# Optimization experiments

Hardware: AMD Instinct MI355X
Metric: run time of the kernel (lower is better)

## Reference

```python
import jax, jax.numpy as jnp
import numpy as np

N, E, G = 100000, 1600000, 500
F_IN, H, OUT, MD = 128, 128, 1, 30


def gcn_conv(x, src, dst, ew, W, b):
    # PyG GCNConv: x' = D^-1/2 (A + I) D^-1/2 (x W) + b, with edge weights ew
    n = x.shape[0]
    h = x @ W  # [N, H]
    loops = jnp.arange(n)
    s = jnp.concatenate([src, loops])
    d = jnp.concatenate([dst, loops])
    w = jnp.concatenate([ew, jnp.ones((n,), dtype=x.dtype)])
    deg = jax.ops.segment_sum(w, d, num_segments=n)
    dinv = jnp.where(deg > 0, jax.lax.rsqrt(deg), 0.0).astype(x.dtype)
    norm = dinv[s] * w * dinv[d]  # [E+N]
    out = jax.ops.segment_sum(norm[:, None] * h[s], d, num_segments=n)
    return out + b


def setup_inputs() -> dict:
    key = jax.random.key(0)
    ks = jax.random.split(key, 12)
    x = jax.random.normal(ks[0], (N, F_IN), dtype=jnp.float32)
    edge_index = jax.random.randint(ks[1], (2, E), 0, N, dtype=jnp.int64)
    edge_attr = jax.random.uniform(ks[2], (E,), dtype=jnp.float32)
    batch = jnp.sort(jax.random.randint(ks[3], (N,), 0, G, dtype=jnp.int64))
    metadata = jax.random.normal(ks[4], (G, MD), dtype=jnp.float32)
    s = lambda fi, fo: 1.0 / np.sqrt(fi)
    W1 = jax.random.normal(ks[5], (F_IN, H), dtype=jnp.float32) * s(F_IN, H)
    b1 = jnp.zeros((H,), dtype=jnp.float32)
    W2 = jax.random.normal(ks[6], (H, H), dtype=jnp.float32) * s(H, H)
    b2 = jnp.zeros((H,), dtype=jnp.float32)
    Wm = jax.random.normal(ks[7], (MD, H), dtype=jnp.float32) * s(MD, H)
    bm = jnp.zeros((H,), dtype=jnp.float32)
    Wf = jax.random.normal(ks[8], (2 * H, OUT), dtype=jnp.float32) * s(2 * H, OUT)
    bf = jnp.zeros((OUT,), dtype=jnp.float32)
    return {"x": x, "edge_index": edge_index, "edge_attr": edge_attr,
            "batch": batch, "metadata": metadata,
            "W1": W1, "b1": b1, "W2": W2, "b2": b2,
            "Wm": Wm, "bm": bm, "Wf": Wf, "bf": bf}


def reference(x, edge_index, edge_attr, batch, metadata, W1, b1, W2, b2, Wm, bm, Wf, bf):
    src, dst = edge_index[0], edge_index[1]
    h = jax.nn.relu(gcn_conv(x, src, dst, edge_attr, W1, b1))
    h = jax.nn.relu(gcn_conv(h, src, dst, edge_attr, W2, b2))
    # global_mean_pool over batch ids
    sums = jax.ops.segment_sum(h, batch, num_segments=G)
    cnt = jax.ops.segment_sum(jnp.ones((h.shape[0],), h.dtype), batch, num_segments=G)
    pooled = sums / jnp.maximum(cnt, 1.0)[:, None]  # [G, H]
    # per-graph metadata: first node index of graph i, idx = first_node % M
    first_node = jax.ops.segment_min(jnp.arange(batch.shape[0]), batch, num_segments=G)
    idx = first_node % metadata.shape[0]
    md = metadata[idx]  # [G, MD]
    md = jax.nn.relu(md @ Wm + bm)  # dropout inactive at eval
    z = jnp.concatenate([pooled, md], axis=1)
    return z @ Wf + bf
```

## Files before the change

kernel.cpp:

```cpp
#include <hip/hip_runtime.h>
#include <cstdint>


#define BK_SHIFT 9
#define BK_NODES 512
#define CH 4096
#define NODE_BITS 17
#define NODE_MASK ((1 << NODE_BITS) - 1)

typedef short bf16x8 __attribute__((ext_vector_type(8)));
typedef float f32x4 __attribute__((ext_vector_type(4)));

union bfpack {
    uint4 u;
    bf16x8 b;
};

static __device__ __forceinline__ unsigned int f2bf(float f) {
    unsigned int u = __float_as_uint(f);
    return (u + 0x7fffu + ((u >> 16) & 1u)) >> 16;
}
static __device__ __forceinline__ unsigned int packbf2(float a, float b) {
    return f2bf(a) | (f2bf(b) << 16);
}
static __device__ __forceinline__ float bf_lo(unsigned int v) {
    return __uint_as_float(v << 16);
}
static __device__ __forceinline__ float bf_hi(unsigned int v) {
    return __uint_as_float(v & 0xffff0000u);
}

__global__ void k_init_small(int* gstart, int* gend, int G, int* bcnt, int NBK) {
    int g = blockIdx.x * blockDim.x + threadIdx.x;
    if (g < G) { gstart[g] = 0x7fffffff; gend[g] = 0; }
    if (g < NBK) bcnt[g] = 0;
}

__global__ void k_init_nodes(const int* __restrict__ batch,
                             int* __restrict__ gstart, int* __restrict__ gend, int N) {
    int i = blockIdx.x * blockDim.x + threadIdx.x;
    if (i >= N) return;
    int b = batch[i];
    if (i == 0 || batch[i - 1] != b) gstart[b] = i;
    if (i == N - 1 || batch[i + 1] != b) gend[b] = i + 1;
}

__global__ __launch_bounds__(256) void k_binhist(const int* __restrict__ dst, int E,
                                                 int* __restrict__ bcnt, int NBK) {
    __shared__ int h[256];
    int tid = threadIdx.x;
    h[tid] = 0;
    __syncthreads();
    int base = blockIdx.x * CH;
    int nend = min(base + CH, E);
    for (int i = base + tid; i < nend; i += 256) atomicAdd(&h[dst[i] >> BK_SHIFT], 1);
    __syncthreads();
    if (tid < NBK && h[tid]) atomicAdd(&bcnt[tid], h[tid]);
}

__global__ __launch_bounds__(256) void k_binscan(const int* __restrict__ bcnt,
                                                 int* __restrict__ bbase,
                                                 int* __restrict__ bfill, int NBK) {
    __shared__ int sc[256];
    int tid = threadIdx.x;
    int v = (tid < NBK) ? bcnt[tid] : 0;
    sc[tid] = v;
    __syncthreads();
    for (int d = 1; d < 256; d <<= 1) {
        int t = (tid >= d) ? sc[tid - d] : 0;
        __syncthreads();
        sc[tid] += t;
        __syncthreads();
    }
    int excl = sc[tid] - v;
    if (tid < NBK) { bbase[tid] = excl; bfill[tid] = excl; }
    if (tid == 255) bbase[NBK] = sc[255];
}

__global__ __launch_bounds__(256) void k_binscatter(const int* __restrict__ src,
                                                    const int* __restrict__ dst,
                                                    const float* __restrict__ ew,
                                                    int* __restrict__ bfill,
                                                    int2* __restrict__ binned, int E) {
    __shared__ int2 stage2[CH];
    __shared__ unsigned char bkt2[CH];
    __shared__ int hist[256], sc[256], lofs[256], cnt2[256], gbase[256];
    int tid = threadIdx.x;
    int base = blockIdx.x * CH;
    int n = min(CH, E - base);
    hist[tid] = 0;
    cnt2[tid] = 0;
    __syncthreads();
    int2 ev[CH / 256];
    int bk[CH / 256];
#pragma unroll
    for (int j = 0; j < CH / 256; ++j) {
        int i = base + tid + j * 256;
        bk[j] = -1;
        if (i < base + n) {
            int s = src[i], d = dst[i];
            float w = ew[i];
            int b = d >> BK_SHIFT;
            ev[j] = make_int2(s | ((d & (BK_NODES - 1)) << NODE_BITS), __float_as_int(w));
            bk[j] = b;
            atomicAdd(&hist[b], 1);
        }
    }
    __syncthreads();
    int hv = hist[tid];
    sc[tid] = hv;
    __syncthreads();
    for (int d = 1; d < 256; d <<= 1) {
        int t = (tid >= d) ? sc[tid - d] : 0;
        __syncthreads();
        sc[tid] += t;
        __syncthreads();
    }
    lofs[tid] = sc[tid] - hv;
    gbase[tid] = hv ? atomicAdd(&bfill[tid], hv) : 0;
    __syncthreads();
#pragma unroll
    for (int j = 0; j < CH / 256; ++j) {
        if (bk[j] >= 0) {
            int r = atomicAdd(&cnt2[bk[j]], 1);
            int p = lofs[bk[j]] + r;
            stage2[p] = ev[j];
            bkt2[p] = (unsigned char)bk[j];
        }
    }
    __syncthreads();
    for (int i = tid; i < n; i += 256) {
        int b = bkt2[i];
        binned[gbase[b] + (i - lofs[b])] = stage2[i];
    }
}

__global__ __launch_bounds__(256) void k_csr(const int2* __restrict__ binned,
                                             const int* __restrict__ bbase,
                                             int2* __restrict__ cvb,
                                             int* __restrict__ rowptr,
                                             float* __restrict__ dinv, int N, int E) {
    __shared__ int lh[BK_NODES];
    __shared__ float ls[BK_NODES];
    __shared__ int lofs[BK_NODES];
    __shared__ int s2[256];
    int tid = threadIdx.x;
    int b = blockIdx.x;
    int nbase = b << BK_SHIFT;
    int nend = min(nbase + BK_NODES, N);
    int ebase = bbase[b], eend = bbase[b + 1];
    for (int i = tid; i < BK_NODES; i += 256) { lh[i] = 0; ls[i] = 0.f; }
    __syncthreads();
    for (int e = ebase + tid; e < eend; e += 256) {
        int2 v = binned[e];
        int local = (v.x >> NODE_BITS) & (BK_NODES - 1);
        atomicAdd(&lh[local], 1);
        atomicAdd(&ls[local], __int_as_float(v.y));
    }
    __syncthreads();
    int p0 = lh[2 * tid], p1 = lh[2 * tid + 1];
    int pv = p0 + p1;
    s2[tid] = pv;
    __syncthreads();
    for (int d = 1; d < 256; d <<= 1) {
        int t = (tid >= d) ? s2[tid - d] : 0;
        __syncthreads();
        s2[tid] += t;
        __syncthreads();
    }
    int e2 = s2[tid] - pv;
    lofs[2 * tid] = e2;
    lofs[2 * tid + 1] = e2 + p0;
    __syncthreads();
    for (int i = nbase + tid; i < nend; i += 256) {
        int local = i - nbase;
        rowptr[i] = ebase + lofs[local];
        dinv[i] = rsqrtf(1.0f + ls[local]);
    }
    if (b == 0 && tid == 0) rowptr[N] = E;
    __syncthreads();
    for (int e = ebase + tid; e < eend; e += 256) {
        int2 v = binned[e];
        int local = (v.x >> NODE_BITS) & (BK_NODES - 1);
        int r = atomicAdd(&lofs[local], 1);
        cvb[ebase + r] = make_int2(v.x & NODE_MASK, v.y);
    }
}

__global__ __launch_bounds__(256) void k_wtboth(const float* __restrict__ W1,
                                                const float* __restrict__ W2,
                                                unsigned short* __restrict__ WT1,
                                                unsigned short* __restrict__ WT2) {
    int idx = blockIdx.x * 256 + threadIdx.x;
    const float* W = (idx < 16384) ? W1 : W2;
    unsigned short* WT = (idx < 16384) ? WT1 : WT2;
    int i = idx & 16383;
    int n = i >> 7, k = i & 127;
    WT[i] = (unsigned short)f2bf(W[(size_t)k * 128 + n]);
}

__global__ __launch_bounds__(256) void k_gemm1(const float* __restrict__ X,
                                               const unsigned short* __restrict__ WT,
                                               const float* __restrict__ dinv,
                                               unsigned short* __restrict__ Y, int M) {
    int tid = threadIdx.x;
    int wid = tid >> 6, lane = tid & 63;
    int rowb = blockIdx.x * 64 + wid * 16;
    int r16 = lane & 15, kg = lane >> 4;
    int arow = min(rowb + r16, M - 1);
    const float* xr = X + (size_t)arow * 128 + kg * 8;
    bf16x8 a[4];
#pragma unroll
    for (int kc = 0; kc < 4; ++kc) {
        float4 u = *reinterpret_cast<const float4*>(xr + kc * 32);
        float4 v = *reinterpret_cast<const float4*>(xr + kc * 32 + 4);
        bfpack pk;
        pk.u = make_uint4(packbf2(u.x, u.y), packbf2(u.z, u.w),
                          packbf2(v.x, v.y), packbf2(v.z, v.w));
        a[kc] = pk.b;
    }
    float dv[4];
#pragma unroll
    for (int r = 0; r < 4; ++r) {
        int ro = rowb + kg * 4 + r;
        dv[r] = (ro < M) ? dinv[ro] : 0.f;
    }
    const bf16x8* Bp = reinterpret_cast<const bf16x8*>(WT + (size_t)r16 * 128 + kg * 8);
#pragma unroll
    for (int nt = 0; nt < 8; ++nt) {
        const bf16x8* B = Bp + (size_t)nt * 256;
        f32x4 acc = {0.f, 0.f, 0.f, 0.f};
        acc = __builtin_amdgcn_mfma_f32_16x16x32_bf16(a[0], B[0], acc, 0, 0, 0);
        acc = __builtin_amdgcn_mfma_f32_16x16x32_bf16(a[1], B[4], acc, 0, 0, 0);
        acc = __builtin_amdgcn_mfma_f32_16x16x32_bf16(a[2], B[8], acc, 0, 0, 0);
        acc = __builtin_amdgcn_mfma_f32_16x16x32_bf16(a[3], B[12], acc, 0, 0, 0);
        int colo = nt * 16 + r16;
#pragma unroll
        for (int r = 0; r < 4; ++r) {
            int ro = rowb + kg * 4 + r;
            if (ro < M) Y[(size_t)ro * 128 + colo] = (unsigned short)f2bf(acc[r] * dv[r]);
        }
    }
}

__global__ __launch_bounds__(256) void k_aggemm(const uint2* __restrict__ Hb2,
                                                const int* __restrict__ rowptr,
                                                const int2* __restrict__ cvb,
                                                const float* __restrict__ dinv,
                                                const float* __restrict__ bias,
                                                const unsigned short* __restrict__ WT2,
                                                unsigned short* __restrict__ Y, int N) {
    __shared__ int2 lcv[4][4][2][64];
    __shared__ uint2 hst[32][33];
    int tid = threadIdx.x;
    int lane = tid & 63, wid = tid >> 6;
    int half = lane >> 5, sl = lane & 31;
    int blockbase = blockIdx.x * 32;
    int n0 = blockbase + wid * 8;
    bool active = (n0 < N);
    float a[4][4];
#pragma unroll
    for (int s = 0; s < 4; ++s)
#pragma unroll
        for (int q = 0; q < 4; ++q) a[s][q] = 0.f;
    if (active) {
        int rv = rowptr[min(n0 + min(lane, 8), N)];
        int rp[9];
#pragma unroll
        for (int k = 0; k < 9; ++k) rp[k] = __shfl(rv, k);
        int cnt[8];
        int nmax = 0;
#pragma unroll
        for (int k = 0; k < 8; ++k) {
            cnt[k] = rp[k + 1] - rp[k];
            nmax = max(nmax, cnt[k]);
        }
#pragma unroll
        for (int s = 0; s < 4; ++s) {
            int ns = n0 + 2 * s + half;
            uint2 hv = (ns < N) ? Hb2[(size_t)ns * 32 + sl] : make_uint2(0u, 0u);
            a[s][0] = bf_lo(hv.x);
            a[s][1] = bf_hi(hv.x);
            a[s][2] = bf_lo(hv.y);
            a[s][3] = bf_hi(hv.y);
        }
        for (int base = 0; base < nmax; base += 64) {
#pragma unroll
            for (int s = 0; s < 4; ++s) {
#pragma unroll
                for (int h = 0; h < 2; ++h) {
                    int k = 2 * s + h;
                    int2 t = (base + lane < cnt[k]) ? cvb[rp[k] + base + lane]
                                                    : make_int2(0, 0);
                    lcv[wid][s][h][lane] = t;
                }
            }
            int m = min(64, nmax - base);
            for (int j0 = 0; j0 < m; j0 += 8) {
#pragma unroll
                for (int jj = 0; jj < 8; ++jj) {
                    int j = j0 + jj;
                    if (j < m) {
                        int2 e0 = lcv[wid][0][half][j];
                        int2 e1 = lcv[wid][1][half][j];
                        int2 e2 = lcv[wid][2][half][j];
                        int2 e3 = lcv[wid][3][half][j];
                        uint2 h0 = Hb2[(size_t)e0.x * 32 + sl];
                        uint2 h1 = Hb2[(size_t)e1.x * 32 + sl];
                        uint2 h2 = Hb2[(size_t)e2.x * 32 + sl];
                        uint2 h3 = Hb2[(size_t)e3.x * 32 + sl];
                        float w0 = __int_as_float(e0.y);
                        float w1 = __int_as_float(e1.y);
                        float w2 = __int_as_float(e2.y);
                        float w3 = __int_as_float(e3.y);
                        a[0][0] = fmaf(w0, bf_lo(h0.x), a[0][0]);
                        a[0][1] = fmaf(w0, bf_hi(h0.x), a[0][1]);
                        a[0][2] = fmaf(w0, bf_lo(h0.y), a[0][2]);
                        a[0][3] = fmaf(w0, bf_hi(h0.y), a[0][3]);
                        a[1][0] = fmaf(w1, bf_lo(h1.x), a[1][0]);
                        a[1][1] = fmaf(w1, bf_hi(h1.x), a[1][1]);
                        a[1][2] = fmaf(w1, bf_lo(h1.y), a[1][2]);
                        a[1][3] = fmaf(w1, bf_hi(h1.y), a[1][3]);
                        a[2][0] = fmaf(w2, bf_lo(h2.x), a[2][0]);
                        a[2][1] = fmaf(w2, bf_hi(h2.x), a[2][1]);
                        a[2][2] = fmaf(w2, bf_lo(h2.y), a[2][2]);
                        a[2][3] = fmaf(w2, bf_hi(h2.y), a[2][3]);
                        a[3][0] = fmaf(w3, bf_lo(h3.x), a[3][0]);
                        a[3][1] = fmaf(w3, bf_hi(h3.x), a[3][1]);
                        a[3][2] = fmaf(w3, bf_lo(h3.y), a[3][2]);
                        a[3][3] = fmaf(w3, bf_hi(h3.y), a[3][3]);
                    }
                }
            }
        }
    }
    float4 bv = reinterpret_cast<const float4*>(bias)[sl];
#pragma unroll
    for (int s = 0; s < 4; ++s) {
        int ns = n0 + 2 * s + half;
        uint2 o = make_uint2(0u, 0u);
        if (active && ns < N) {
            float d = dinv[ns];
            float o0 = fmaxf(fmaf(a[s][0], d, bv.x), 0.f);
            float o1 = fmaxf(fmaf(a[s][1], d, bv.y), 0.f);
            float o2 = fmaxf(fmaf(a[s][2], d, bv.z), 0.f);
            float o3 = fmaxf(fmaf(a[s][3], d, bv.w), 0.f);
            o = make_uint2(packbf2(o0, o1), packbf2(o2, o3));
        }
        hst[wid * 8 + 2 * s + half][sl] = o;
    }
    __syncthreads();
    int r16 = lane & 15, kg = lane >> 4;
    int trow = wid >> 1;
    int ntb = (wid & 1) * 4;
    int arow = trow * 16 + r16;
    bf16x8 afr[4];
#pragma unroll
    for (int kc = 0; kc < 4; ++kc) {
        uint2 lo = hst[arow][kc * 8 + kg * 2];
        uint2 hi = hst[arow][kc * 8 + kg * 2 + 1];
        bfpack pk;
        pk.u = make_uint4(lo.x, lo.y, hi.x, hi.y);
        afr[kc] = pk.b;
    }
    float dv[4];
#pragma unroll
    for (int r = 0; r < 4; ++r) {
        int ro = blockbase + trow * 16 + kg * 4 + r;
        dv[r] = (ro < N) ? dinv[ro] : 0.f;
    }
    const bf16x8* Bp = reinterpret_cast<const bf16x8*>(WT2 + (size_t)r16 * 128 + kg * 8);
#pragma unroll
    for (int nt = 0; nt < 4; ++nt) {
        const bf16x8* B = Bp + (size_t)(ntb + nt) * 256;
        f32x4 acc = {0.f, 0.f, 0.f, 0.f};
        acc = __builtin_amdgcn_mfma_f32_16x16x32_bf16(afr[0], B[0], acc, 0, 0, 0);
        acc = __builtin_amdgcn_mfma_f32_16x16x32_bf16(afr[1], B[4], acc, 0, 0, 0);
        acc = __builtin_amdgcn_mfma_f32_16x16x32_bf16(afr[2], B[8], acc, 0, 0, 0);
        acc = __builtin_amdgcn_mfma_f32_16x16x32_bf16(afr[3], B[12], acc, 0, 0, 0);
        int colo = (ntb + nt) * 16 + r16;
#pragma unroll
        for (int r = 0; r < 4; ++r) {
            int ro = blockbase + trow * 16 + kg * 4 + r;
            if (ro < N) Y[(size_t)ro * 128 + colo] = (unsigned short)f2bf(acc[r] * dv[r]);
        }
    }
}

__global__ __launch_bounds__(256) void k_agg(const uint2* __restrict__ Hb2,
                                             const int* __restrict__ rowptr,
                                             const int2* __restrict__ cvb,
                                             const float* __restrict__ dinv,
                                             const float* __restrict__ bias,
                                             uint2* __restrict__ OutB2, int N) {
    __shared__ int2 lcv[4][4][2][64];
    int tid = threadIdx.x;
    int lane = tid & 63, wid = tid >> 6;
    int half = lane >> 5, sl = lane & 31;
    int n0 = (blockIdx.x * 4 + wid) * 8;
    if (n0 >= N) return;
    int rv = rowptr[min(n0 + min(lane, 8), N)];
    int rp[9];
#pragma unroll
    for (int k = 0; k < 9; ++k) rp[k] = __shfl(rv, k);
    int cnt[8];
    int nmax = 0;
#pragma unroll
    for (int k = 0; k < 8; ++k) {
        cnt[k] = rp[k + 1] - rp[k];
        nmax = max(nmax, cnt[k]);
    }
    float a[4][4];
#pragma unroll
    for (int s = 0; s < 4; ++s) {
        int ns = n0 + 2 * s + half;
        uint2 hv = (ns < N) ? Hb2[(size_t)ns * 32 + sl] : make_uint2(0u, 0u);
        a[s][0] = bf_lo(hv.x);
        a[s][1] = bf_hi(hv.x);
        a[s][2] = bf_lo(hv.y);
        a[s][3] = bf_hi(hv.y);
    }
    for (int base = 0; base < nmax; base += 64) {
#pragma unroll
        for (int s = 0; s < 4; ++s) {
#pragma unroll
            for (int h = 0; h < 2; ++h) {
                int k = 2 * s + h;
                int2 t = (base + lane < cnt[k]) ? cvb[rp[k] + base + lane]
                                                : make_int2(0, 0);
                lcv[wid][s][h][lane] = t;
            }
        }
        int m = min(64, nmax - base);
        for (int j0 = 0; j0 < m; j0 += 8) {
#pragma unroll
            for (int jj = 0; jj < 8; ++jj) {
                int j = j0 + jj;
                if (j < m) {
                    int2 e0 = lcv[wid][0][half][j];
                    int2 e1 = lcv[wid][1][half][j];
                    int2 e2 = lcv[wid][2][half][j];
                    int2 e3 = lcv[wid][3][half][j];
                    uint2 h0 = Hb2[(size_t)e0.x * 32 + sl];
                    uint2 h1 = Hb2[(size_t)e1.x * 32 + sl];
                    uint2 h2 = Hb2[(size_t)e2.x * 32 + sl];
                    uint2 h3 = Hb2[(size_t)e3.x * 32 + sl];
                    float w0 = __int_as_float(e0.y);
                    float w1 = __int_as_float(e1.y);
                    float w2 = __int_as_float(e2.y);
                    float w3 = __int_as_float(e3.y);
                    a[0][0] = fmaf(w0, bf_lo(h0.x), a[0][0]);
                    a[0][1] = fmaf(w0, bf_hi(h0.x), a[0][1]);
                    a[0][2] = fmaf(w0, bf_lo(h0.y), a[0][2]);
                    a[0][3] = fmaf(w0, bf_hi(h0.y), a[0][3]);
                    a[1][0] = fmaf(w1, bf_lo(h1.x), a[1][0]);
                    a[1][1] = fmaf(w1, bf_hi(h1.x), a[1][1]);
                    a[1][2] = fmaf(w1, bf_lo(h1.y), a[1][2]);
                    a[1][3] = fmaf(w1, bf_hi(h1.y), a[1][3]);
                    a[2][0] = fmaf(w2, bf_lo(h2.x), a[2][0]);
                    a[2][1] = fmaf(w2, bf_hi(h2.x), a[2][1]);
                    a[2][2] = fmaf(w2, bf_lo(h2.y), a[2][2]);
                    a[2][3] = fmaf(w2, bf_hi(h2.y), a[2][3]);
                    a[3][0] = fmaf(w3, bf_lo(h3.x), a[3][0]);
                    a[3][1] = fmaf(w3, bf_hi(h3.x), a[3][1]);
                    a[3][2] = fmaf(w3, bf_lo(h3.y), a[3][2]);
                    a[3][3] = fmaf(w3, bf_hi(h3.y), a[3][3]);
                }
            }
        }
    }
    float4 bv = reinterpret_cast<const float4*>(bias)[sl];
#pragma unroll
    for (int s = 0; s < 4; ++s) {
        int ns = n0 + 2 * s + half;
        if (ns < N) {
            float d = dinv[ns];
            float o0 = fmaxf(fmaf(a[s][0], d, bv.x), 0.f);
            float o1 = fmaxf(fmaf(a[s][1], d, bv.y), 0.f);
            float o2 = fmaxf(fmaf(a[s][2], d, bv.z), 0.f);
            float o3 = fmaxf(fmaf(a[s][3], d, bv.w), 0.f);
            OutB2[(size_t)ns * 32 + sl] = make_uint2(packbf2(o0, o1), packbf2(o2, o3));
        }
    }
}

__global__ __launch_bounds__(256) void k_poolhead(const unsigned int* __restrict__ H2u,
                                                  const int* __restrict__ gstart,
                                                  const int* __restrict__ gend,
                                                  const float* __restrict__ meta,
                                                  const float* __restrict__ Wm,
                                                  const float* __restrict__ bm,
                                                  const float* __restrict__ Wf,
                                                  const float* __restrict__ bf,
                                                  float* __restrict__ out, int G) {
    int g = blockIdx.x;
    int tid = threadIdx.x;
    int cu = tid & 63, q = tid >> 6;
    __shared__ float r0[256], r1[256];
    __shared__ float pooled[128];
    __shared__ float red[128];
    int b = gstart[g];
    int e = gend[g];
    int cntg = e - b;
    float s0 = 0.f, s1 = 0.f;
    for (int i = q; i < cntg; i += 4) {
        unsigned int v = H2u[(size_t)(b + i) * 64 + cu];
        s0 += bf_lo(v);
        s1 += bf_hi(v);
    }
    r0[tid] = s0; r1[tid] = s1;
    __syncthreads();
    if (tid < 64) {
        float t0 = r0[cu] + r0[cu + 64] + r0[cu + 128] + r0[cu + 192];
        float t1 = r1[cu] + r1[cu + 64] + r1[cu + 128] + r1[cu + 192];
        float inv = 1.f / fmaxf((float)cntg, 1.f);
        pooled[2 * cu] = t0 * inv;
        pooled[2 * cu + 1] = t1 * inv;
    }
    __syncthreads();
    if (tid < 128) {
        int c = tid;
        int idx = gstart[g] % G;
        float m = bm[c];
#pragma unroll
        for (int k = 0; k < 30; ++k) m = fmaf(meta[idx * 30 + k], Wm[k * 128 + c], m);
        m = fmaxf(m, 0.f);
        red[c] = pooled[c] * Wf[c] + m * Wf[128 + c];
    }
    __syncthreads();
    for (int st = 64; st > 0; st >>= 1) {
        if (tid < st) red[tid] += red[tid + st];
        __syncthreads();
    }
    if (tid == 0) out[g] = red[0] + bf[0];
}

extern "C" void kernel_launch(void* const* d_in, const int* in_sizes, int n_in,
                              void* d_out, int out_size, void* d_ws, size_t ws_size,
                              hipStream_t stream) {
    const float* x     = (const float*)d_in[0];
    const int*   ei    = (const int*)d_in[1];
    const float* ew    = (const float*)d_in[2];
    const int*   batch = (const int*)d_in[3];
    const float* meta  = (const float*)d_in[4];
    const float* W1    = (const float*)d_in[5];
    const float* b1    = (const float*)d_in[6];
    const float* W2    = (const float*)d_in[7];
    const float* b2    = (const float*)d_in[8];
    const float* Wm    = (const float*)d_in[9];
    const float* bm    = (const float*)d_in[10];
    const float* Wf    = (const float*)d_in[11];
    const float* bf    = (const float*)d_in[12];

    int N = in_sizes[0] / 128;
    int E = in_sizes[2];
    int G = in_sizes[4] / 30;
    int Mpad = (N + 63) & ~63;
    int NBK = (N + BK_NODES - 1) >> BK_SHIFT;
    const int* srcp = ei;
    const int* dstp = ei + E;

    char* p = (char*)d_ws;
    auto alloc = [&](size_t bytes) -> void* {
        void* r = p;
        p += (bytes + 255) & ~(size_t)255;
        return r;
    };
    float* dinv   = (float*)alloc((size_t)N * 4);
    int*   rowptr = (int*)alloc((size_t)(N + 1) * 4);
    int2*  binned = (int2*)alloc((size_t)E * 8);
    int2*  cvb    = (int2*)alloc((size_t)E * 8);
    int*   bcnt   = (int*)alloc((size_t)NBK * 4);
    int*   bbase  = (int*)alloc((size_t)(NBK + 1) * 4);
    int*   bfillp = (int*)alloc((size_t)NBK * 4);
    unsigned short* H   = (unsigned short*)alloc((size_t)Mpad * 128 * 2);
    unsigned short* H2  = (unsigned short*)alloc((size_t)Mpad * 128 * 2);
    unsigned short* WT1 = (unsigned short*)alloc(128 * 128 * 2);
    unsigned short* WT2 = (unsigned short*)alloc(128 * 128 * 2);
    int*   gstart = (int*)alloc((size_t)G * 4);
    int*   gend   = (int*)alloc((size_t)G * 4);

    int EB = (E + CH - 1) / CH;
    k_init_small<<<(max(G, NBK) + 255) / 256, 256, 0, stream>>>(gstart, gend, G, bcnt, NBK);
    k_init_nodes<<<(N + 255) / 256, 256, 0, stream>>>(batch, gstart, gend, N);
    k_binhist<<<EB, 256, 0, stream>>>(dstp, E, bcnt, NBK);
    k_binscan<<<1, 256, 0, stream>>>(bcnt, bbase, bfillp, NBK);
    k_binscatter<<<EB, 256, 0, stream>>>(srcp, dstp, ew, bfillp, binned, E);
    k_csr<<<NBK, 256, 0, stream>>>(binned, bbase, cvb, rowptr, dinv, N, E);

    k_wtboth<<<128, 256, 0, stream>>>(W1, W2, WT1, WT2);

    k_gemm1<<<Mpad / 64, 256, 0, stream>>>(x, WT1, dinv, H, N);
    int NB32 = (N + 31) / 32;
    k_aggemm<<<NB32, 256, 0, stream>>>((const uint2*)H, rowptr, cvb, dinv, b1, WT2,
                                       H2, N);
    k_agg<<<NB32, 256, 0, stream>>>((const uint2*)H2, rowptr, cvb, dinv, b2,
                                    (uint2*)H, N);

    k_poolhead<<<G, 256, 0, stream>>>((const unsigned int*)H, gstart, gend,
                                      meta, Wm, bm, Wf, bf, (float*)d_out, G);
}
```

Baseline: 290.9 us.

## Make fused aggregate-GEMM per-wave to drop block barrier; privatize histogram per wave

The fused aggregation+GEMM kernel now has each wave work independently: it stages its own 8 rows in a per-wave shared buffer, reused for both edge lists and output staging, and runs the 16x16 MFMA with half the rows zero-padded over all 8 column tiles. This removes the __syncthreads and lets waves with no work exit early, so one slow wave no longer holds the others up. In exchange, half of every MFMA's work is wasted on padding and each wave issues twice as many MFMAs. The bin histogram also gets per-wave shared-memory copies to cut atomic contention.

```diff
diff --git a/kernel.cpp b/kernel.cpp
--- a/kernel.cpp
+++ b/kernel.cpp
@@ -47,15 +47,20 @@
 
 __global__ __launch_bounds__(256) void k_binhist(const int* __restrict__ dst, int E,
                                                  int* __restrict__ bcnt, int NBK) {
-    __shared__ int h[256];
-    int tid = threadIdx.x;
-    h[tid] = 0;
+    __shared__ int h[4][256];
+    int tid = threadIdx.x;
+    int wid = tid >> 6;
+#pragma unroll
+    for (int w = 0; w < 4; ++w) h[w][tid & 255] = 0;
     __syncthreads();
     int base = blockIdx.x * CH;
     int nend = min(base + CH, E);
-    for (int i = base + tid; i < nend; i += 256) atomicAdd(&h[dst[i] >> BK_SHIFT], 1);
-    __syncthreads();
-    if (tid < NBK && h[tid]) atomicAdd(&bcnt[tid], h[tid]);
+    for (int i = base + tid; i < nend; i += 256) atomicAdd(&h[wid][dst[i] >> BK_SHIFT], 1);
+    __syncthreads();
+    if (tid < NBK) {
+        int s = h[0][tid] + h[1][tid] + h[2][tid] + h[3][tid];
+        if (s) atomicAdd(&bcnt[tid], s);
+    }
 }
 
 __global__ __launch_bounds__(256) void k_binscan(const int* __restrict__ bcnt,
@@ -250,86 +255,80 @@
                                                 const float* __restrict__ bias,
                                                 const unsigned short* __restrict__ WT2,
                                                 unsigned short* __restrict__ Y, int N) {
-    __shared__ int2 lcv[4][4][2][64];
-    __shared__ uint2 hst[32][33];
+    __shared__ int2 smbuf[4][512];
     int tid = threadIdx.x;
     int lane = tid & 63, wid = tid >> 6;
     int half = lane >> 5, sl = lane & 31;
-    int blockbase = blockIdx.x * 32;
-    int n0 = blockbase + wid * 8;
-    bool active = (n0 < N);
+    int2 (*lcv)[2][64] = reinterpret_cast<int2(*)[2][64]>(&smbuf[wid][0]);
+    uint2 (*hst)[33]   = reinterpret_cast<uint2(*)[33]>(&smbuf[wid][0]);
+    int n0 = (blockIdx.x * 4 + wid) * 8;
+    if (n0 >= N) return;
+    int rv = rowptr[min(n0 + min(lane, 8), N)];
+    int rp[9];
+#pragma unroll
+    for (int k = 0; k < 9; ++k) rp[k] = __shfl(rv, k);
+    int cnt[8];
+    int nmax = 0;
+#pragma unroll
+    for (int k = 0; k < 8; ++k) {
+        cnt[k] = rp[k + 1] - rp[k];
+        nmax = max(nmax, cnt[k]);
+    }
     float a[4][4];
 #pragma unroll
-    for (int s = 0; s < 4; ++s)
-#pragma unroll
-        for (int q = 0; q < 4; ++q) a[s][q] = 0.f;
-    if (active) {
-        int rv = rowptr[min(n0 + min(lane, 8), N)];
-        int rp[9];
-#pragma unroll
-        for (int k = 0; k < 9; ++k) rp[k] = __shfl(rv, k);
-        int cnt[8];
-        int nmax = 0;
-#pragma unroll
-        for (int k = 0; k < 8; ++k) {
-            cnt[k] = rp[k + 1] - rp[k];
-            nmax = max(nmax, cnt[k]);
-        }
+    for (int s = 0; s < 4; ++s) {
+        int ns = n0 + 2 * s + half;
+        uint2 hv = (ns < N) ? Hb2[(size_t)ns * 32 + sl] : make_uint2(0u, 0u);
+        a[s][0] = bf_lo(hv.x);
+        a[s][1] = bf_hi(hv.x);
+        a[s][2] = bf_lo(hv.y);
+        a[s][3] = bf_hi(hv.y);
+    }
+    for (int base = 0; base < nmax; base += 64) {
 #pragma unroll
         for (int s = 0; s < 4; ++s) {
-            int ns = n0 + 2 * s + half;
-            uint2 hv = (ns < N) ? Hb2[(size_t)ns * 32 + sl] : make_uint2(0u, 0u);
-            a[s][0] = bf_lo(hv.x);
-            a[s][1] = bf_hi(hv.x);
-            a[s][2] = bf_lo(hv.y);
-            a[s][3] = bf_hi(hv.y);
-        }
-        for (int base = 0; base < nmax; base += 64) {
-#pragma unroll
-            for (int s = 0; s < 4; ++s) {
-#pragma unroll
-                for (int h = 0; h < 2; ++h) {
-                    int k = 2 * s + h;
-                    int2 t = (base + lane < cnt[k]) ? cvb[rp[k] + base + lane]
-                                                    : make_int2(0, 0);
-                    lcv[wid][s][h][lane] = t;
-                }
+#pragma unroll
+            for (int h = 0; h < 2; ++h) {
+                int k = 2 * s + h;
+                int2 t = (base + lane < cnt[k]) ? cvb[rp[k] + base + lane]
+                                                : make_int2(0, 0);
+                lcv[s][h][lane] = t;
             }
-            int m = min(64, nmax - base);
-            for (int j0 = 0; j0 < m; j0 += 8) {
-#pragma unroll
-                for (int jj = 0; jj < 8; ++jj) {
-                    int j = j0 + jj;
-                    if (j < m) {
-                        int2 e0 = lcv[wid][0][half][j];
-                        int2 e1 = lcv[wid][1][half][j];
-                        int2 e2 = lcv[wid][2][half][j];
-                        int2 e3 = lcv[wid][3][half][j];
-                        uint2 h0 = Hb2[(size_t)e0.x * 32 + sl];
-                        uint2 h1 = Hb2[(size_t)e1.x * 32 + sl];
-                        uint2 h2 = Hb2[(size_t)e2.x * 32 + sl];
-                        uint2 h3 = Hb2[(size_t)e3.x * 32 + sl];
-                        float w0 = __int_as_float(e0.y);
-                        float w1 = __int_as_float(e1.y);
-                        float w2 = __int_as_float(e2.y);
-                        float w3 = __int_as_float(e3.y);
-                        a[0][0] = fmaf(w0, bf_lo(h0.x), a[0][0]);
-                        a[0][1] = fmaf(w0, bf_hi(h0.x), a[0][1]);
-                        a[0][2] = fmaf(w0, bf_lo(h0.y), a[0][2]);
-                        a[0][3] = fmaf(w0, bf_hi(h0.y), a[0][3]);
-                        a[1][0] = fmaf(w1, bf_lo(h1.x), a[1][0]);
-                        a[1][1] = fmaf(w1, bf_hi(h1.x), a[1][1]);
-                        a[1][2] = fmaf(w1, bf_lo(h1.y), a[1][2]);
-                        a[1][3] = fmaf(w1, bf_hi(h1.y), a[1][3]);
-                        a[2][0] = fmaf(w2, bf_lo(h2.x), a[2][0]);
-                        a[2][1] = fmaf(w2, bf_hi(h2.x), a[2][1]);
-                        a[2][2] = fmaf(w2, bf_lo(h2.y), a[2][2]);
-                        a[2][3] = fmaf(w2, bf_hi(h2.y), a[2][3]);
-                        a[3][0] = fmaf(w3, bf_lo(h3.x), a[3][0]);
-                        a[3][1] = fmaf(w3, bf_hi(h3.x), a[3][1]);
-                        a[3][2] = fmaf(w3, bf_lo(h3.y), a[3][2]);
-                        a[3][3] = fmaf(w3, bf_hi(h3.y), a[3][3]);
-                    }
+        }
+        int m = min(64, nmax - base);
+        for (int j0 = 0; j0 < m; j0 += 8) {
+#pragma unroll
+            for (int jj = 0; jj < 8; ++jj) {
+                int j = j0 + jj;
+                if (j < m) {
+                    int2 e0 = lcv[0][half][j];
+                    int2 e1 = lcv[1][half][j];
+                    int2 e2 = lcv[2][half][j];
+                    int2 e3 = lcv[3][half][j];
+                    uint2 h0 = Hb2[(size_t)e0.x * 32 + sl];
+                    uint2 h1 = Hb2[(size_t)e1.x * 32 + sl];
+                    uint2 h2 = Hb2[(size_t)e2.x * 32 + sl];
+                    uint2 h3 = Hb2[(size_t)e3.x * 32 + sl];
+                    float w0 = __int_as_float(e0.y);
+                    float w1 = __int_as_float(e1.y);
+                    float w2 = __int_as_float(e2.y);
+                    float w3 = __int_as_float(e3.y);
+                    a[0][0] = fmaf(w0, bf_lo(h0.x), a[0][0]);
+                    a[0][1] = fmaf(w0, bf_hi(h0.x), a[0][1]);
+                    a[0][2] = fmaf(w0, bf_lo(h0.y), a[0][2]);
+                    a[0][3] = fmaf(w0, bf_hi(h0.y), a[0][3]);
+                    a[1][0] = fmaf(w1, bf_lo(h1.x), a[1][0]);
+                    a[1][1] = fmaf(w1, bf_hi(h1.x), a[1][1]);
+                    a[1][2] = fmaf(w1, bf_lo(h1.y), a[1][2]);
+                    a[1][3] = fmaf(w1, bf_hi(h1.y), a[1][3]);
+                    a[2][0] = fmaf(w2, bf_lo(h2.x), a[2][0]);
+                    a[2][1] = fmaf(w2, bf_hi(h2.x), a[2][1]);
+                    a[2][2] = fmaf(w2, bf_lo(h2.y), a[2][2]);
+                    a[2][3] = fmaf(w2, bf_hi(h2.y), a[2][3]);
+                    a[3][0] = fmaf(w3, bf_lo(h3.x), a[3][0]);
+                    a[3][1] = fmaf(w3, bf_hi(h3.x), a[3][1]);
+                    a[3][2] = fmaf(w3, bf_lo(h3.y), a[3][2]);
+                    a[3][3] = fmaf(w3, bf_hi(h3.y), a[3][3]);
                 }
             }
         }
@@ -339,7 +338,7 @@
     for (int s = 0; s < 4; ++s) {
         int ns = n0 + 2 * s + half;
         uint2 o = make_uint2(0u, 0u);
-        if (active && ns < N) {
+        if (ns < N) {
             float d = dinv[ns];
             float o0 = fmaxf(fmaf(a[s][0], d, bv.x), 0.f);
             float o1 = fmaxf(fmaf(a[s][1], d, bv.y), 0.f);
@@ -347,42 +346,45 @@
             float o3 = fmaxf(fmaf(a[s][3], d, bv.w), 0.f);
             o = make_uint2(packbf2(o0, o1), packbf2(o2, o3));
         }
-        hst[wid * 8 + 2 * s + half][sl] = o;
-    }
-    __syncthreads();
+        hst[2 * s + half][sl] = o;
+    }
     int r16 = lane & 15, kg = lane >> 4;
-    int trow = wid >> 1;
-    int ntb = (wid & 1) * 4;
-    int arow = trow * 16 + r16;
     bf16x8 afr[4];
 #pragma unroll
     for (int kc = 0; kc < 4; ++kc) {
-        uint2 lo = hst[arow][kc * 8 + kg * 2];
-        uint2 hi = hst[arow][kc * 8 + kg * 2 + 1];
         bfpack pk;
-        pk.u = make_uint4(lo.x, lo.y, hi.x, hi.y);
+        pk.u = make_uint4(0u, 0u, 0u, 0u);
+        if (r16 < 8) {
+            uint2 lo = hst[r16][kc * 8 + kg * 2];
+            uint2 hi = hst[r16][kc * 8 + kg * 2 + 1];
+            pk.u = make_uint4(lo.x, lo.y, hi.x, hi.y);
+        }
         afr[kc] = pk.b;
     }
     float dv[4];
 #pragma unroll
     for (int r = 0; r < 4; ++r) {
-        int ro = blockbase + trow * 16 + kg * 4 + r;
-        dv[r] = (ro < N) ? dinv[ro] : 0.f;
+        int row = kg * 4 + r;
+        int ro = n0 + row;
+        dv[r] = (row < 8 && ro < N) ? dinv[ro] : 0.f;
     }
     const bf16x8* Bp = reinterpret_cast<const bf16x8*>(WT2 + (size_t)r16 * 128 + kg * 8);
 #pragma unroll
-    for (int nt = 0; nt < 4; ++nt) {
-        const bf16x8* B = Bp + (size_t)(ntb + nt) * 256;
+    for (int nt = 0; nt < 8; ++nt) {
+        const bf16x8* B = Bp + (size_t)nt * 256;
         f32x4 acc = {0.f, 0.f, 0.f, 0.f};
         acc = __builtin_amdgcn_mfma_f32_16x16x32_bf16(afr[0], B[0], acc, 0, 0, 0);
         acc = __builtin_amdgcn_mfma_f32_16x16x32_bf16(afr[1], B[4], acc, 0, 0, 0);
         acc = __builtin_amdgcn_mfma_f32_16x16x32_bf16(afr[2], B[8], acc, 0, 0, 0);
         acc = __builtin_amdgcn_mfma_f32_16x16x32_bf16(afr[3], B[12], acc, 0, 0, 0);
-        int colo = (ntb + nt) * 16 + r16;
+        int colo = nt * 16 + r16;
 #pragma unroll
         for (int r = 0; r < 4; ++r) {
-            int ro = blockbase + trow * 16 + kg * 4 + r;
-            if (ro < N) Y[(size_t)ro * 128 + colo] = (unsigned short)f2bf(acc[r] * dv[r]);
+            int row = kg * 4 + r;
+            if (row < 8) {
+                int ro = n0 + row;
+                if (ro < N) Y[(size_t)ro * 128 + colo] = (unsigned short)f2bf(acc[r] * dv[r]);
+            }
         }
     }
 }
```

Measured after the change: 314.0 us. 8.0% more time.
